# Kernel optimization log

Hardware: AMD Instinct MI355X
Metric: run time of the kernel (lower is better)

## Reference

```python
import jax, jax.numpy as jnp
import numpy as np

N, E, B, P = 131072, 262144, 4096, 1024
HID, CTX, FEAT, L = 256, 128, 512, 4


def _ln(x, g, bb, eps=1e-5):
    mu = jnp.mean(x, -1, keepdims=True)
    v = jnp.mean((x - mu) ** 2, -1, keepdims=True)
    return (x - mu) * jax.lax.rsqrt(v + eps) * g + bb


def setup_inputs() -> dict:
    key = jax.random.key(0)
    ks = iter(jax.random.split(key, 64))
    nrm = lambda sh, s=0.05: (jax.random.normal(next(ks), sh, jnp.float32) * s)
    inp = {
        "nf": jax.random.normal(next(ks), (N, 69), jnp.float32),
        "ei": jax.random.randint(next(ks), (2, E), 0, N, dtype=jnp.int32),
        "ef": jax.random.normal(next(ks), (E, 9), jnp.float32),
        "b": jnp.sort(jax.random.randint(next(ks), (N,), 0, B, dtype=jnp.int32)),
        "pid": jax.random.randint(next(ks), (B,), 0, P, dtype=jnp.int32),
        # MPNN params
        "Wn": nrm((69, HID)), "bn": jnp.zeros((HID,)),
        "We": nrm((9, HID)), "be": jnp.zeros((HID,)),
        "Wm": nrm((L, 2 * HID, HID)), "bm": jnp.zeros((L, HID)),
        "Wu": nrm((L, HID, HID)), "bu": jnp.zeros((L, HID)),
        "lng": jnp.ones((L, HID)), "lnb": jnp.zeros((L, HID)),
        # context embedding
        "ctx_emb": nrm((P, CTX), 0.02),
        # FiLM gamma net: Linear(128,256)-LN-ReLU-Linear(256,512)
        "gW1": nrm((CTX, HID)), "gb1": jnp.zeros((HID,)),
        "glng": jnp.ones((HID,)), "glnb": jnp.zeros((HID,)),
        "gW2": nrm((HID, FEAT)), "gb2": jnp.ones((FEAT,)),
        # FiLM beta net
        "bW1": nrm((CTX, HID)), "bb1": jnp.zeros((HID,)),
        "blng": jnp.ones((HID,)), "blnb": jnp.zeros((HID,)),
        "bW2": nrm((HID, FEAT)), "bb2": jnp.zeros((FEAT,)),
        # predictor: Linear(512,256)-ReLU-Linear(256,1)
        "pW1": nrm((FEAT, HID)), "pb1": jnp.zeros((HID,)),
        "pW2": nrm((HID, 1)), "pb2": jnp.zeros((1,)),
    }
    return inp


def reference(nf, ei, ef, b, pid, Wn, bn, We, be, Wm, bm, Wu, bu, lng, lnb,
              ctx_emb, gW1, gb1, glng, glnb, gW2, gb2,
              bW1, bb1, blng, blnb, bW2, bb2, pW1, pb1, pW2, pb2):
    src, dst = ei[0], ei[1]
    h = jax.nn.relu(nf @ Wn + bn)          # [N,256]
    e = jax.nn.relu(ef @ We + be)          # [E,256]
    for l in range(L):
        m = jax.nn.relu(jnp.concatenate([h[src], e], -1) @ Wm[l] + bm[l])  # [E,256]
        agg = jax.ops.segment_sum(m, dst, num_segments=N)                   # scatter-add
        h = _ln(h + jax.nn.relu(agg @ Wu[l] + bu[l]), lng[l], lnb[l])
    # graph readout: mean || max -> [B,512]
    ssum = jax.ops.segment_sum(h, b, num_segments=B)
    cnt = jnp.maximum(jax.ops.segment_sum(jnp.ones((h.shape[0], 1), h.dtype), b, num_segments=B), 1.0)
    gmax = jax.ops.segment_max(h, b, num_segments=B)
    gmax = jnp.where(jnp.isneginf(gmax), 0.0, gmax)
    g = jnp.concatenate([ssum / cnt, gmax], -1)  # [B,512]
    # FiLM fusion
    c = ctx_emb[pid]                              # [B,128]
    gamma = jax.nn.relu(_ln(c @ gW1 + gb1, glng, glnb)) @ gW2 + gb2
    beta = jax.nn.relu(_ln(c @ bW1 + bb1, blng, blnb)) @ bW2 + bb2
    hmod = gamma * g + beta
    out = (jax.nn.relu(hmod @ pW1 + pb1) @ pW2 + pb2).squeeze(-1)  # [B]
    return out
```

## Files before the change

### kernel.cpp

```cpp
#include <hip/hip_runtime.h>
#include <hip/hip_bf16.h>
#include <math.h>

#define HID 256
#define CTXD 128
#define FEAT 512
#define NLAYER 4

#define SW(n) (((n) >> 1) & 3)

typedef __hip_bfloat16 bf16;
typedef __attribute__((ext_vector_type(8))) short short8;
typedef __attribute__((ext_vector_type(4))) float floatx4;

__device__ __forceinline__ float bf2f(bf16 x) { return __bfloat162float(x); }
__device__ __forceinline__ bf16 f2bf(float x) { return __float2bfloat16(x); }
__device__ __forceinline__ float us2f(unsigned short u) {
    union { unsigned u; float f; } c; c.u = ((unsigned)u) << 16; return c.f;
}
__device__ __forceinline__ unsigned short f2us(float f) {
    bf16 b = f2bf(f); return *(unsigned short*)&b;
}

__device__ __forceinline__ void glds16(const void* g, void* l) {
    __builtin_amdgcn_global_load_lds(
        (__attribute__((address_space(1))) void*)g,
        (__attribute__((address_space(3))) void*)l, 16, 0, 0);
}

__global__ __launch_bounds__(256) void hist_kernel(const int* __restrict__ dst,
                                                   int* __restrict__ cnt, int E)
{
    int i = blockIdx.x * 256 + threadIdx.x;
    if (i < E) atomicAdd(&cnt[dst[i]], 1);
}

__global__ __launch_bounds__(256) void scan1_kernel(int* __restrict__ cnt,
                                                    int* __restrict__ bsum)
{
    __shared__ int sd[256];
    const int t = threadIdx.x;
    const int i = blockIdx.x * 256 + t;
    int v = cnt[i];
    sd[t] = v;
    __syncthreads();
    for (int o = 1; o < 256; o <<= 1) {
        int x = (t >= o) ? sd[t - o] : 0;
        __syncthreads();
        sd[t] += x;
        __syncthreads();
    }
    cnt[i] = sd[t] - v;
    if (t == 255) bsum[blockIdx.x] = sd[255];
}

__global__ void scan2_kernel(int* __restrict__ bsum)
{
    __shared__ int sd[512];
    const int t = threadIdx.x;
    int v = bsum[t];
    sd[t] = v;
    __syncthreads();
    for (int o = 1; o < 512; o <<= 1) {
        int x = (t >= o) ? sd[t - o] : 0;
        __syncthreads();
        sd[t] += x;
        __syncthreads();
    }
    bsum[t] = sd[t] - v;
}

__global__ __launch_bounds__(256) void scan3_kernel(int* __restrict__ cnt,
                                                    const int* __restrict__ bsum)
{
    int i = blockIdx.x * 256 + threadIdx.x;
    cnt[i] += bsum[blockIdx.x];
}

__global__ __launch_bounds__(256) void scatter_perm_kernel(
    const int* __restrict__ dst, int* __restrict__ cursor,
    int* __restrict__ perm, int E)
{
    int i = blockIdx.x * 256 + threadIdx.x;
    if (i < E) {
        int p = atomicAdd(&cursor[dst[i]], 1);
        perm[p] = i;
    }
}

__global__ __launch_bounds__(256)
void build_wimg_kernel(const float* __restrict__ W, bf16* __restrict__ img,
                       int K, int KT, int L)
{
    long idx = (long)blockIdx.x * 256 + threadIdx.x;
    long tot = (long)L * KT * 8192;
    if (idx >= tot) return;
    int l  = (int)(idx / ((long)KT * 8192));
    int r  = (int)(idx % ((long)KT * 8192));
    int kt = r >> 13;
    int r2 = r & 8191;
    int n  = r2 >> 5;
    int s  = (r2 >> 3) & 3;
    int j  = r2 & 7;
    int k  = kt * 32 + ((s ^ SW(n)) * 8) + j;
    float v = (k < K) ? W[((long)l * K + k) * HID + n] : 0.f;
    img[idx] = f2bf(v);
}

__device__ __forceinline__ void kt_tail512(
    int kt, const bf16* __restrict__ Wimg, const float* __restrict__ W,
    short* As, short* Bs, floatx4 (&acc)[4][4])
{
    const int t = threadIdx.x;
    const int w = t >> 6, lane = t & 63;
    const int fr = lane & 15, q = lane >> 4;
    const int wm = (w & 1) * 64, wn = (w >> 1) * 64;
    const int k0 = kt * 32;

    if (Wimg) {
        const short* base = (const short*)Wimg + (long)kt * 8192;
#pragma unroll
        for (int j = 0; j < 2; ++j) {
            const int chunk = w * 2 + j;
            glds16(base + chunk * 512 + lane * 8, (char*)Bs + chunk * 1024);
        }
    } else {
#pragma unroll
        for (int cc = 0; cc < 2; ++cc) {
            const int slot = t + cc * 512;
            const int n    = slot >> 2;
            const int kg   = slot & 3;
            const int kk   = k0 + kg * 8;
            short8 pk;
#pragma unroll
            for (int j = 0; j < 8; ++j)
                pk[j] = (short)f2us(W[(long)(kk + j) * HID + n]);
            *(short8*)&Bs[n * 32 + (kg ^ SW(n)) * 8] = pk;
        }
    }
    __syncthreads();
    short8 af[4], bf8[4];
#pragma unroll
    for (int mt = 0; mt < 4; ++mt) {
        const int r = wm + mt * 16 + fr;
        af[mt] = *(const short8*)&As[r * 32 + (q ^ SW(r)) * 8];
    }
#pragma unroll
    for (int nt = 0; nt < 4; ++nt) {
        const int r = wn + nt * 16 + fr;
        bf8[nt] = *(const short8*)&Bs[r * 32 + (q ^ SW(r)) * 8];
    }
#pragma unroll
    for (int mt = 0; mt < 4; ++mt)
#pragma unroll
        for (int nt = 0; nt < 4; ++nt)
            acc[mt][nt] = __builtin_amdgcn_mfma_f32_16x16x32_bf16(
                af[mt], bf8[nt], acc[mt][nt], 0, 0, 0);
    __syncthreads();
}

__device__ __forceinline__ void kt_tail256(
    int kt, const bf16* __restrict__ Wimg, const float* __restrict__ W,
    short* As, short* Bs, floatx4 (&acc)[4][4])
{
    const int t = threadIdx.x;
    const int w = t >> 6, lane = t & 63;
    const int fr = lane & 15, q = lane >> 4;
    const int wn = w * 64;
    const int k0 = kt * 32;

    if (Wimg) {
        const short* base = (const short*)Wimg + (long)kt * 8192;
#pragma unroll
        for (int j = 0; j < 4; ++j) {
            const int chunk = w * 4 + j;
            glds16(base + chunk * 512 + lane * 8, (char*)Bs + chunk * 1024);
        }
    } else {
#pragma unroll
        for (int cc = 0; cc < 4; ++cc) {
            const int slot = t + cc * 256;
            const int n    = slot >> 2;
            const int kg   = slot & 3;
            const int kk   = k0 + kg * 8;
            short8 pk;
#pragma unroll
            for (int j = 0; j < 8; ++j)
                pk[j] = (short)f2us(W[(long)(kk + j) * HID + n]);
            *(short8*)&Bs[n * 32 + (kg ^ SW(n)) * 8] = pk;
        }
    }
    __syncthreads();
    short8 af[4], bf8[4];
#pragma unroll
    for (int mt = 0; mt < 4; ++mt) {
        const int r = mt * 16 + fr;
        af[mt] = *(const short8*)&As[r * 32 + (q ^ SW(r)) * 8];
    }
#pragma unroll
    for (int nt = 0; nt < 4; ++nt) {
        const int r = wn + nt * 16 + fr;
        bf8[nt] = *(const short8*)&Bs[r * 32 + (q ^ SW(r)) * 8];
    }
#pragma unroll
    for (int mt = 0; mt < 4; ++mt)
#pragma unroll
        for (int nt = 0; nt < 4; ++nt)
            acc[mt][nt] = __builtin_amdgcn_mfma_f32_16x16x32_bf16(
                af[mt], bf8[nt], acc[mt][nt], 0, 0, 0);
    __syncthreads();
}

__global__ __launch_bounds__(512)
void ht_gemm(const bf16* __restrict__ h_, const float* __restrict__ W,
             const bf16* __restrict__ Wimg, bf16* __restrict__ ht)
{
    __shared__ __align__(16) short As[128 * 32];
    __shared__ __align__(16) short Bs[256 * 32];

    const int  t  = threadIdx.x;
    const long bm = (long)blockIdx.x * 128;

    floatx4 acc[4][4];
#pragma unroll
    for (int i = 0; i < 4; ++i)
#pragma unroll
        for (int j = 0; j < 4; ++j) acc[i][j] = (floatx4){0.f, 0.f, 0.f, 0.f};

    const int w = t >> 6, lane = t & 63;
    const int fr = lane & 15, q = lane >> 4;
    const int wm = (w & 1) * 64, wn = (w >> 1) * 64;
    const int arow = t >> 2, akg = t & 3;
    const int aslot = arow * 32 + (akg ^ SW(arow)) * 8;

    for (int kt = 0; kt < 8; ++kt) {
        const int kk = kt * 32 + akg * 8;
        short8 v = *(const short8*)((const short*)h_ + (bm + arow) * HID + kk);
        *(short8*)&As[aslot] = v;
        kt_tail512(kt, Wimg, W, As, Bs, acc);
    }

#pragma unroll
    for (int nt = 0; nt < 4; ++nt) {
        const int col = wn + nt * 16 + fr;
#pragma unroll
        for (int mt = 0; mt < 4; ++mt)
#pragma unroll
            for (int reg = 0; reg < 4; ++reg) {
                const long row = bm + wm + mt * 16 + q * 4 + reg;
                ht[row * HID + col] = f2bf(acc[mt][nt][reg]);
            }
    }
}

__global__ __launch_bounds__(256)
void msg_agg(const bf16* __restrict__ ht, const float* __restrict__ ef,
             const float* __restrict__ We, const float* __restrict__ be,
             const int* __restrict__ src, const int* __restrict__ perm,
             const int* __restrict__ cursor,
             const float* __restrict__ W, const bf16* __restrict__ Wimg,
             const float* __restrict__ bias, bf16* __restrict__ agg)
{
    __shared__ __align__(16) short As[64 * 32];
    __shared__ __align__(16) short Bs[256 * 32];
    __shared__ __align__(16) short htL[64 * 256];
    __shared__ int   rpL[65];
    __shared__ int   srcL[64];
    __shared__ int   edgeL[64];
    __shared__ float efL[64][9];

    const int t  = threadIdx.x;
    const int n0 = blockIdx.x * 64;

    if (t < 64) rpL[t + 1] = cursor[n0 + t];
    if (t == 0) rpL[0] = (n0 == 0) ? 0 : cursor[n0 - 1];
    __syncthreads();
    const int j0 = rpL[0], j1 = rpL[64];
    int nch = (j1 - j0 + 63) >> 6;
    if (nch < 1) nch = 1;

    const int w = t >> 6, lane = t & 63;
    const int fr = lane & 15, q = lane >> 4;
    const int wn = w * 64;
    const int arow = t >> 2, akg = t & 3;
    const int aslot = arow * 32 + (akg ^ SW(arow)) * 8;
    const int srow = t >> 2, ssg = t & 3;

    for (int ch = 0; ch < nch; ++ch) {
        const int jc = j0 + ch * 64;
        if (t < 64) {
            const int j = jc + t;
            const int eg = (j < j1) ? perm[j] : 0;
            edgeL[t] = eg;
            srcL[t]  = src[eg];
        }
        __syncthreads();
        for (int i = t; i < 64 * 9; i += 256) {
            const int r = i / 9, qq = i % 9;
            efL[r][qq] = (jc + r < j1) ? ef[(long)edgeL[r] * 9 + qq] : 0.f;
        }
        short8 stash[8];
        {
            const short* hp = (const short*)ht + (long)srcL[srow] * HID + ssg * 64;
#pragma unroll
            for (int i = 0; i < 8; ++i) stash[i] = *(const short8*)(hp + i * 8);
        }
        __syncthreads();

        floatx4 acc[4][4];
#pragma unroll
        for (int i = 0; i < 4; ++i)
#pragma unroll
            for (int j = 0; j < 4; ++j) acc[i][j] = (floatx4){0.f, 0.f, 0.f, 0.f};

        for (int kt = 0; kt < 8; ++kt) {
            const int kc = kt * 32 + akg * 8;
            float sv[8];
#pragma unroll
            for (int j = 0; j < 8; ++j) sv[j] = be[kc + j];
#pragma unroll
            for (int qq = 0; qq < 9; ++qq) {
                const float efv = efL[arow][qq];
#pragma unroll
                for (int j = 0; j < 8; ++j)
                    sv[j] = fmaf(efv, We[qq * HID + kc + j], sv[j]);
            }
            short8 pk;
#pragma unroll
            for (int j = 0; j < 8; ++j) pk[j] = (short)f2us(fmaxf(sv[j], 0.f));
            *(short8*)&As[aslot] = pk;
            kt_tail256(kt, Wimg, W, As, Bs, acc);
        }

        {
            short* hl = &htL[srow * 256 + ssg * 64];
#pragma unroll
            for (int i = 0; i < 8; ++i) *(short8*)(hl + i * 8) = stash[i];
        }
        __syncthreads();

#pragma unroll
        for (int nt = 0; nt < 4; ++nt) {
            const int col = wn + nt * 16 + fr;
            const float bv = bias[col];
#pragma unroll
            for (int mt = 0; mt < 4; ++mt)
#pragma unroll
                for (int reg = 0; reg < 4; ++reg) {
                    const int rl = mt * 16 + q * 4 + reg;
                    const float v = fmaxf(acc[mt][nt][reg] + bv +
                                          us2f((unsigned short)htL[rl * 256 + col]), 0.f);
                    htL[rl * 256 + col] = (short)f2us(v);
                }
        }
        __syncthreads();

        for (int nn = 0; nn < 16; ++nn) {
            const int nl = w * 16 + nn;
            int a = rpL[nl]     - jc; if (a < 0)  a = 0;
            int b = rpL[nl + 1] - jc; if (b > 64) b = 64;
            float s0 = 0.f, s1 = 0.f, s2 = 0.f, s3 = 0.f;
            for (int r = a; r < b; ++r) {
                const ushort4 hv = *(const ushort4*)&htL[r * 256 + lane * 4];
                s0 += us2f(hv.x); s1 += us2f(hv.y);
                s2 += us2f(hv.z); s3 += us2f(hv.w);
            }
            bf16* ap = agg + (long)(n0 + nl) * HID + lane * 4;
            if (ch == 0) {
                unsigned short o[4] = {f2us(s0), f2us(s1), f2us(s2), f2us(s3)};
                *(ushort4*)ap = *(const ushort4*)o;
            } else if (b > a) {
                const ushort4 ov = *(const ushort4*)ap;
                unsigned short o[4] = {f2us(s0 + us2f(ov.x)), f2us(s1 + us2f(ov.y)),
                                       f2us(s2 + us2f(ov.z)), f2us(s3 + us2f(ov.w))};
                *(ushort4*)ap = *(const ushort4*)o;
            }
        }
        __syncthreads();
    }
}

__global__ __launch_bounds__(512)
void upd_gemm5(const bf16* __restrict__ agg,
               const float* __restrict__ W, const bf16* __restrict__ Wimg,
               const float* __restrict__ bias,
               const float* __restrict__ lng, const float* __restrict__ lnb,
               bf16* __restrict__ h_)
{
    __shared__ __align__(16) short As[128 * 32];
    __shared__ __align__(16) short Bs[256 * 32];
    __shared__ float redS[128][4];
    __shared__ float redS2[128][4];

    const int  t  = threadIdx.x;
    const long bm = (long)blockIdx.x * 128;

    floatx4 acc[4][4];
#pragma unroll
    for (int i = 0; i < 4; ++i)
#pragma unroll
        for (int j = 0; j < 4; ++j) acc[i][j] = (floatx4){0.f, 0.f, 0.f, 0.f};

    const int w = t >> 6, lane = t & 63;
    const int fr = lane & 15, q = lane >> 4;
    const int wm = (w & 1) * 64, wn = (w >> 1) * 64;
    const int arow = t >> 2, akg = t & 3;
    const int aslot = arow * 32 + (akg ^ SW(arow)) * 8;

    for (int kt = 0; kt < 8; ++kt) {
        const int kk = kt * 32 + akg * 8;
        short8 v = *(const short8*)((const short*)agg + (bm + arow) * HID + kk);
        *(short8*)&As[aslot] = v;
        kt_tail512(kt, Wimg, W, As, Bs, acc);
    }

    const int wnIdx = w >> 1;
#pragma unroll
    for (int mt = 0; mt < 4; ++mt)
#pragma unroll
        for (int reg = 0; reg < 4; ++reg) {
            const int  lrow = wm + mt * 16 + q * 4 + reg;
            const long row  = bm + lrow;
            float ps = 0.f, ps2 = 0.f;
#pragma unroll
            for (int nt = 0; nt < 4; ++nt) {
                const int col = wn + nt * 16 + fr;
                float v = bf2f(h_[row * HID + col]) +
                          fmaxf(acc[mt][nt][reg] + bias[col], 0.f);
                acc[mt][nt][reg] = v;
                ps  += v;
                ps2 += v * v;
            }
#pragma unroll
            for (int m = 1; m < 16; m <<= 1) {
                ps  += __shfl_xor(ps, m);
                ps2 += __shfl_xor(ps2, m);
            }
            if (fr == 0) { redS[lrow][wnIdx] = ps; redS2[lrow][wnIdx] = ps2; }
        }
    __syncthreads();
#pragma unroll
    for (int mt = 0; mt < 4; ++mt)
#pragma unroll
        for (int reg = 0; reg < 4; ++reg) {
            const int  lrow = wm + mt * 16 + q * 4 + reg;
            const long row  = bm + lrow;
            const float ts  = redS[lrow][0] + redS[lrow][1] +
                              redS[lrow][2] + redS[lrow][3];
            const float ts2 = redS2[lrow][0] + redS2[lrow][1] +
                              redS2[lrow][2] + redS2[lrow][3];
            const float mu  = ts * (1.f / 256.f);
            const float var = ts2 * (1.f / 256.f) - mu * mu;
            const float rs  = rsqrtf(var + 1e-5f);
#pragma unroll
            for (int nt = 0; nt < 4; ++nt) {
                const int col = wn + nt * 16 + fr;
                const float y = (acc[mt][nt][reg] - mu) * rs * lng[col] + lnb[col];
                h_[row * HID + col] = f2bf(y);
            }
        }
}

__global__ __launch_bounds__(512)
void enc_gemm3(const float* __restrict__ nf, const bf16* __restrict__ Wimg,
               const float* __restrict__ bias, bf16* __restrict__ h_)
{
    __shared__ __align__(16) short As[128 * 32];
    __shared__ __align__(16) short Bs[256 * 32];

    const int  t  = threadIdx.x;
    const long bm = (long)blockIdx.x * 128;

    floatx4 acc[4][4];
#pragma unroll
    for (int i = 0; i < 4; ++i)
#pragma unroll
        for (int j = 0; j < 4; ++j) acc[i][j] = (floatx4){0.f, 0.f, 0.f, 0.f};

    const int w = t >> 6, lane = t & 63;
    const int fr = lane & 15, q = lane >> 4;
    const int wm = (w & 1) * 64, wn = (w >> 1) * 64;
    const int arow = t >> 2, akg = t & 3;
    const int aslot = arow * 32 + (akg ^ SW(arow)) * 8;

    for (int kt = 0; kt < 3; ++kt) {
        const int kk = kt * 32 + akg * 8;
        short8 pk;
#pragma unroll
        for (int j = 0; j < 8; ++j) {
            const int k = kk + j;
            pk[j] = (short)f2us((k < 69) ? nf[(bm + arow) * 69 + k] : 0.f);
        }
        *(short8*)&As[aslot] = pk;
        kt_tail512(kt, Wimg, nullptr, As, Bs, acc);
    }

#pragma unroll
    for (int nt = 0; nt < 4; ++nt) {
        const int col = wn + nt * 16 + fr;
        const float bv = bias[col];
#pragma unroll
        for (int mt = 0; mt < 4; ++mt)
#pragma unroll
            for (int reg = 0; reg < 4; ++reg) {
                const long row = bm + wm + mt * 16 + q * 4 + reg;
                h_[row * HID + col] = f2bf(fmaxf(acc[mt][nt][reg] + bv, 0.f));
            }
    }
}

struct PlainF32 {
    const float* A; int lda;
    __device__ float operator()(int r, int k) const { return A[(long)r * lda + k]; }
};
struct CtxF32 {
    const float* ctx; const int* pid;
    __device__ float operator()(int r, int k) const {
        return ctx[(long)pid[r] * CTXD + k];
    }
};
struct StoreF32 {
    float* C; int ldc; int relu;
    __device__ void operator()(int r, int c, const float* v) const {
        float4 o;
        o.x = v[0]; o.y = v[1]; o.z = v[2]; o.w = v[3];
        if (relu) {
            o.x = fmaxf(o.x, 0.f); o.y = fmaxf(o.y, 0.f);
            o.z = fmaxf(o.z, 0.f); o.w = fmaxf(o.w, 0.f);
        }
        *(float4*)&C[(long)r * ldc + c] = o;
    }
};
struct StoreBf16Relu {
    bf16* C;
    __device__ void operator()(int r, int c, const float* v) const {
        bf16 tmp[4];
#pragma unroll
        for (int j = 0; j < 4; ++j) tmp[j] = f2bf(fmaxf(v[j], 0.f));
        *(ushort4*)&C[(long)r * HID + c] = *(const ushort4*)tmp;
    }
};

template <typename Loader, typename Epi>
__global__ __launch_bounds__(256)
void gemm_tiled(Loader loader, const float* __restrict__ W,
                const float* __restrict__ bias, Epi epi, int M, int K, int Nc)
{
    constexpr int BM = 64, BN = 64, BK = 16;
    __shared__ __align__(16) float As[BK][BM + 4];
    __shared__ __align__(16) float Ws[BK][BN];

    const int bm = blockIdx.x * BM;
    const int bn = blockIdx.y * BN;
    const int t  = threadIdx.x;
    const int arow = t >> 2, akq = (t & 3) * 4;
    const int wn = t & 63, wk0 = t >> 6;
    const int tx = t & 15, ty = t >> 4;

    float acc[4][4] = {};
    const int ntiles = (K + BK - 1) / BK;
    for (int kt = 0; kt < ntiles; ++kt) {
        const int k0 = kt * BK;
#pragma unroll
        for (int i = 0; i < 4; ++i) {
            int k = k0 + akq + i;
            As[akq + i][arow] = (k < K) ? loader(bm + arow, k) : 0.f;
        }
#pragma unroll
        for (int i = 0; i < 4; ++i) {
            int kr = wk0 + i * 4;
            int k  = k0 + kr;
            Ws[kr][wn] = (k < K) ? W[(long)k * Nc + bn + wn] : 0.f;
        }
        __syncthreads();
#pragma unroll
        for (int kk = 0; kk < BK; ++kk) {
            float4 a = *(const float4*)&As[kk][ty * 4];
            float4 b = *(const float4*)&Ws[kk][tx * 4];
            float av[4] = {a.x, a.y, a.z, a.w};
            float bv[4] = {b.x, b.y, b.z, b.w};
#pragma unroll
            for (int i = 0; i < 4; ++i)
#pragma unroll
                for (int j = 0; j < 4; ++j) acc[i][j] += av[i] * bv[j];
        }
        __syncthreads();
    }
#pragma unroll
    for (int i = 0; i < 4; ++i) {
        const int row = bm + ty * 4 + i;
        const int col = bn + tx * 4;
        float v[4];
#pragma unroll
        for (int j = 0; j < 4; ++j) v[j] = acc[i][j] + bias[col + j];
        epi(row, col, v);
    }
}

__global__ __launch_bounds__(256)
void ln_f32_relu_kernel(float* __restrict__ x, const float* __restrict__ g,
                        const float* __restrict__ bb)
{
    const long row = blockIdx.x;
    const int  j   = threadIdx.x;
    float v = x[row * HID + j];
    float s = v, s2 = v * v;
#pragma unroll
    for (int o = 32; o > 0; o >>= 1) {
        s  += __shfl_down(s, o);
        s2 += __shfl_down(s2, o);
    }
    __shared__ float red[2][4];
    const int wid = j >> 6, lane = j & 63;
    if (lane == 0) { red[0][wid] = s; red[1][wid] = s2; }
    __syncthreads();
    float ts  = red[0][0] + red[0][1] + red[0][2] + red[0][3];
    float ts2 = red[1][0] + red[1][1] + red[1][2] + red[1][3];
    float mu  = ts * (1.f / 256.f);
    float var = ts2 * (1.f / 256.f) - mu * mu;
    float y = (v - mu) * rsqrtf(var + 1e-5f) * g[j] + bb[j];
    x[row * HID + j] = fmaxf(y, 0.f);
}

__device__ int lower_bound_i(const int* __restrict__ arr, int n, int val)
{
    int lo = 0, hi = n;
    while (lo < hi) {
        int mid = (lo + hi) >> 1;
        if (arr[mid] < val) lo = mid + 1; else hi = mid;
    }
    return lo;
}

__global__ __launch_bounds__(256)
void readout_kernel(const bf16* __restrict__ h, const int* __restrict__ b,
                    float* __restrict__ gout, int Nn)
{
    const int gidx = blockIdx.x;
    const int j    = threadIdx.x;
    const int lo   = lower_bound_i(b, Nn, gidx);
    const int hi   = lower_bound_i(b, Nn, gidx + 1);
    float s = 0.f, mx = -INFINITY;
    for (int n = lo; n < hi; ++n) {
        float v = bf2f(h[(long)n * HID + j]);
        s += v;
        mx = fmaxf(mx, v);
    }
    const int cnt = hi - lo;
    gout[(long)gidx * FEAT + j]       = s / fmaxf((float)cnt, 1.f);
    gout[(long)gidx * FEAT + HID + j] = (cnt > 0) ? mx : 0.f;
}

__global__ __launch_bounds__(256)
void film_mod_kernel(const float* __restrict__ gamma, float* __restrict__ g,
                     const float* __restrict__ beta, int n)
{
    int i = blockIdx.x * 256 + threadIdx.x;
    if (i < n) g[i] = gamma[i] * g[i] + beta[i];
}

__global__ __launch_bounds__(256)
void final_dot_kernel(const float* __restrict__ ph, const float* __restrict__ w,
                      const float* __restrict__ b2, float* __restrict__ out)
{
    const int row  = blockIdx.x * 4 + (threadIdx.x >> 6);
    const int lane = threadIdx.x & 63;
    float s = 0.f;
#pragma unroll
    for (int k = lane; k < HID; k += 64)
        s += ph[(long)row * HID + k] * w[k];
#pragma unroll
    for (int o = 32; o > 0; o >>= 1) s += __shfl_down(s, o);
    if (lane == 0) out[row] = s + b2[0];
}

__global__ void diag_out_kernel(float* out, int n, float wsmb)
{
    int i = blockIdx.x * 256 + threadIdx.x;
    if (i < n) out[i] = (i == 0) ? wsmb : 0.f;
}

extern "C" void kernel_launch(void* const* d_in, const int* in_sizes, int n_in,
                              void* d_out, int out_size, void* d_ws, size_t ws_size,
                              hipStream_t stream)
{
    const int N = 131072, E = 262144, B = 4096;

    const float* nf   = (const float*)d_in[0];
    const int*   ei   = (const int*)  d_in[1];
    const float* ef   = (const float*)d_in[2];
    const int*   bidx = (const int*)  d_in[3];
    const int*   pid  = (const int*)  d_in[4];
    const float* Wn   = (const float*)d_in[5];
    const float* bn   = (const float*)d_in[6];
    const float* We   = (const float*)d_in[7];
    const float* be   = (const float*)d_in[8];
    const float* Wm   = (const float*)d_in[9];
    const float* bm   = (const float*)d_in[10];
    const float* Wu   = (const float*)d_in[11];
    const float* bu   = (const float*)d_in[12];
    const float* lng  = (const float*)d_in[13];
    const float* lnb  = (const float*)d_in[14];
    const float* ctx  = (const float*)d_in[15];
    const float* gW1  = (const float*)d_in[16];
    const float* gb1  = (const float*)d_in[17];
    const float* glng = (const float*)d_in[18];
    const float* glnb = (const float*)d_in[19];
    const float* gW2  = (const float*)d_in[20];
    const float* gb2  = (const float*)d_in[21];
    const float* bW1  = (const float*)d_in[22];
    const float* bb1  = (const float*)d_in[23];
    const float* blng = (const float*)d_in[24];
    const float* blnb = (const float*)d_in[25];
    const float* bW2  = (const float*)d_in[26];
    const float* bb2  = (const float*)d_in[27];
    const float* pW1  = (const float*)d_in[28];
    const float* pb1  = (const float*)d_in[29];
    const float* pW2  = (const float*)d_in[30];
    const float* pb2  = (const float*)d_in[31];

    const int* src = ei;
    const int* dst = ei + E;
    float* out = (float*)d_out;

    const size_t hB    = (size_t)N * HID * sizeof(bf16);
    const size_t htB   = (size_t)N * HID * sizeof(bf16);
    const size_t aggB  = (size_t)N * HID * sizeof(bf16);
    const size_t curB  = (size_t)N * 4;
    const size_t permB = (size_t)E * 4;
    const size_t bsumB = 2048 * 4;
    const size_t wmImgB = (size_t)NLAYER * 16 * 8192 * 2;
    const size_t wuImgB = (size_t)NLAYER * 8  * 8192 * 2;
    const size_t wnImgB = (size_t)3 * 8192 * 2;

    const size_t needBase = hB + htB + aggB + curB + permB + bsumB;
    const size_t needFull = needBase + wmImgB + wuImgB + wnImgB;

    if (ws_size < needBase) {
        diag_out_kernel<<<dim3((B + 255) / 256), dim3(256), 0, stream>>>(
            out, B, (float)(ws_size >> 20));
        return;
    }
    const bool haveImg = ws_size >= needFull;

    char* p = (char*)d_ws;
    bf16* h      = (bf16*)p;  p += hB;
    bf16* ht     = (bf16*)p;  p += htB;
    bf16* agg    = (bf16*)p;  p += aggB;
    int*  cursor = (int*)p;   p += curB;
    int*  perm   = (int*)p;   p += permB;
    int*  bsum   = (int*)p;   p += bsumB;
    bf16* wmImg = nullptr; bf16* wuImg = nullptr; bf16* wnImg = nullptr;
    if (haveImg) {
        wmImg = (bf16*)p; p += wmImgB;
        wuImg = (bf16*)p; p += wuImgB;
        wnImg = (bf16*)p; p += wnImgB;
    }

    float* gbuf  = (float*)ht;
    float* t1    = gbuf  + (long)B * FEAT;
    float* t2    = t1    + (long)B * HID;
    float* gamma = t2    + (long)B * HID;
    float* beta  = gamma + (long)B * FEAT;
    float* ph    = beta  + (long)B * FEAT;

    dim3 blk(256), blk5(512);

    hipMemsetAsync(cursor, 0, curB, stream);
    hist_kernel<<<dim3(E / 256), blk, 0, stream>>>(dst, cursor, E);
    scan1_kernel<<<dim3(N / 256), blk, 0, stream>>>(cursor, bsum);
    scan2_kernel<<<dim3(1), dim3(512), 0, stream>>>(bsum);
    scan3_kernel<<<dim3(N / 256), blk, 0, stream>>>(cursor, bsum);
    scatter_perm_kernel<<<dim3(E / 256), blk, 0, stream>>>(dst, cursor, perm, E);

    if (haveImg) {
        build_wimg_kernel<<<dim3((NLAYER * 16 * 8192 + 255) / 256), blk, 0, stream>>>(
            Wm, wmImg, 2 * HID, 16, NLAYER);
        build_wimg_kernel<<<dim3((NLAYER * 8 * 8192 + 255) / 256), blk, 0, stream>>>(
            Wu, wuImg, HID, 8, NLAYER);
        build_wimg_kernel<<<dim3((3 * 8192 + 255) / 256), blk, 0, stream>>>(
            Wn, wnImg, 69, 3, 1);
    }

    if (haveImg) {
        enc_gemm3<<<dim3(N / 128), blk5, 0, stream>>>(nf, wnImg, bn, h);
    } else {
        gemm_tiled<<<dim3(N / 64, HID / 64), blk, 0, stream>>>(
            PlainF32{nf, 69}, Wn, bn, StoreBf16Relu{h}, N, 69, HID);
    }

    for (int l = 0; l < NLAYER; ++l) {
        const float* Wml  = Wm  + (long)l * 2 * HID * HID;
        const float* WmlB = Wml + (long)HID * HID;
        const float* bml  = bm  + (long)l * HID;
        const float* Wul  = Wu  + (long)l * HID * HID;
        const float* bul  = bu  + (long)l * HID;
        const float* lngl = lng + (long)l * HID;
        const float* lnbl = lnb + (long)l * HID;
        const bf16* wmTopI = haveImg ? wmImg + (long)l * 16 * 8192 : nullptr;
        const bf16* wmBotI = haveImg ? wmImg + (long)l * 16 * 8192 + 8 * 8192 : nullptr;
        const bf16* wuI    = haveImg ? wuImg + (long)l * 8 * 8192 : nullptr;

        ht_gemm<<<dim3(N / 128), blk5, 0, stream>>>(h, Wml, wmTopI, ht);
        msg_agg<<<dim3(N / 64), blk, 0, stream>>>(
            ht, ef, We, be, src, perm, cursor, WmlB, wmBotI, bml, agg);
        upd_gemm5<<<dim3(N / 128), blk5, 0, stream>>>(
            agg, Wul, wuI, bul, lngl, lnbl, h);
    }

    readout_kernel<<<dim3(B), blk, 0, stream>>>(h, bidx, gbuf, N);

    gemm_tiled<<<dim3(B / 64, HID / 64), blk, 0, stream>>>(
        CtxF32{ctx, pid}, gW1, gb1, StoreF32{t1, HID, 0}, B, CTXD, HID);
    ln_f32_relu_kernel<<<dim3(B), blk, 0, stream>>>(t1, glng, glnb);
    gemm_tiled<<<dim3(B / 64, FEAT / 64), blk, 0, stream>>>(
        PlainF32{t1, HID}, gW2, gb2, StoreF32{gamma, FEAT, 0}, B, HID, FEAT);

    gemm_tiled<<<dim3(B / 64, HID / 64), blk, 0, stream>>>(
        CtxF32{ctx, pid}, bW1, bb1, StoreF32{t2, HID, 0}, B, CTXD, HID);
    ln_f32_relu_kernel<<<dim3(B), blk, 0, stream>>>(t2, blng, blnb);
    gemm_tiled<<<dim3(B / 64, FEAT / 64), blk, 0, stream>>>(
        PlainF32{t2, HID}, bW2, bb2, StoreF32{beta, FEAT, 0}, B, HID, FEAT);

    film_mod_kernel<<<dim3((B * FEAT + 255) / 256), blk, 0, stream>>>(
        gamma, gbuf, beta, B * FEAT);
    gemm_tiled<<<dim3(B / 64, HID / 64), blk, 0, stream>>>(
        PlainF32{gbuf, FEAT}, pW1, pb1, StoreF32{ph, HID, 1}, B, FEAT, HID);
    final_dot_kernel<<<dim3(B / 4), blk, 0, stream>>>(ph, pW2, pb2, out);
}
```

Baseline: 2.146 ms.

## Restructure message kernel to read bottom weights directly from global memory

Adds msg_agg2, which computes the full 64x256 edge-embedding tile into a single swizzled LDS buffer up front. The MFMA loop then runs over all k-tiles, loading B fragments straight from a new plain (unswizzled) bf16 weight image in global/L2, instead of staging weights through LDS with per-k-tile barriers. The shared buffer is then reused for the gathered ht rows and the aggregation. This cuts LDS traffic and synchronisation per chunk, at the cost of register-direct global loads of weights and an extra weight-build kernel.

```diff
diff --git a/kernel.cpp b/kernel.cpp
--- a/kernel.cpp
+++ b/kernel.cpp
@@ -26,6 +26,10 @@
     __builtin_amdgcn_global_load_lds(
         (__attribute__((address_space(1))) void*)g,
         (__attribute__((address_space(3))) void*)l, 16, 0, 0);
+}
+
+__device__ __forceinline__ int hsw(int row, int col) {
+    return row * 256 + ((((col) >> 3) ^ (row & 31)) << 3) + ((col) & 7);
 }
 
 __global__ __launch_bounds__(256) void hist_kernel(const int* __restrict__ dst,
@@ -107,6 +111,23 @@
     img[idx] = f2bf(v);
 }
 
+__global__ __launch_bounds__(256)
+void build_wbot_plain_kernel(const float* __restrict__ Wm, bf16* __restrict__ img)
+{
+    long idx = (long)blockIdx.x * 256 + threadIdx.x;
+    long tot = (long)NLAYER * 8 * 8192;
+    if (idx >= tot) return;
+    int l  = (int)(idx / (8 * 8192));
+    int r  = (int)(idx % (8 * 8192));
+    int kt = r >> 13;
+    int r2 = r & 8191;
+    int n  = r2 >> 5;
+    int kc = r2 & 31;
+    int k  = 256 + kt * 32 + kc;
+    img[(long)l * 16 * 8192 + (long)(8 + kt) * 8192 + n * 32 + kc] =
+        f2bf(Wm[((long)l * 512 + k) * HID + n]);
+}
+
 __device__ __forceinline__ void kt_tail512(
     int kt, const bf16* __restrict__ Wimg, const float* __restrict__ W,
     short* As, short* Bs, floatx4 (&acc)[4][4])
@@ -159,8 +180,195 @@
     __syncthreads();
 }
 
+__global__ __launch_bounds__(512)
+void ht_gemm(const bf16* __restrict__ h_, const float* __restrict__ W,
+             const bf16* __restrict__ Wimg, bf16* __restrict__ ht)
+{
+    __shared__ __align__(16) short As[128 * 32];
+    __shared__ __align__(16) short Bs[256 * 32];
+
+    const int  t  = threadIdx.x;
+    const long bm = (long)blockIdx.x * 128;
+
+    floatx4 acc[4][4];
+#pragma unroll
+    for (int i = 0; i < 4; ++i)
+#pragma unroll
+        for (int j = 0; j < 4; ++j) acc[i][j] = (floatx4){0.f, 0.f, 0.f, 0.f};
+
+    const int w = t >> 6, lane = t & 63;
+    const int fr = lane & 15, q = lane >> 4;
+    const int wm = (w & 1) * 64, wn = (w >> 1) * 64;
+    const int arow = t >> 2, akg = t & 3;
+    const int aslot = arow * 32 + (akg ^ SW(arow)) * 8;
+
+    for (int kt = 0; kt < 8; ++kt) {
+        const int kk = kt * 32 + akg * 8;
+        short8 v = *(const short8*)((const short*)h_ + (bm + arow) * HID + kk);
+        *(short8*)&As[aslot] = v;
+        kt_tail512(kt, Wimg, W, As, Bs, acc);
+    }
+
+#pragma unroll
+    for (int nt = 0; nt < 4; ++nt) {
+        const int col = wn + nt * 16 + fr;
+#pragma unroll
+        for (int mt = 0; mt < 4; ++mt)
+#pragma unroll
+            for (int reg = 0; reg < 4; ++reg) {
+                const long row = bm + wm + mt * 16 + q * 4 + reg;
+                ht[row * HID + col] = f2bf(acc[mt][nt][reg]);
+            }
+    }
+}
+
+__global__ __launch_bounds__(256)
+void msg_agg2(const bf16* __restrict__ ht, const float* __restrict__ ef,
+              const float* __restrict__ We, const float* __restrict__ be,
+              const int* __restrict__ src, const int* __restrict__ perm,
+              const int* __restrict__ cursor,
+              const bf16* __restrict__ WbP,
+              const float* __restrict__ bias, bf16* __restrict__ agg)
+{
+    __shared__ __align__(16) short vL[64 * 256];
+    __shared__ int   rpL[65];
+    __shared__ int   srcL[64];
+    __shared__ int   edgeL[64];
+    __shared__ float efL[64][9];
+
+    const int t  = threadIdx.x;
+    const int n0 = blockIdx.x * 64;
+
+    if (t < 64) rpL[t + 1] = cursor[n0 + t];
+    if (t == 0) rpL[0] = (n0 == 0) ? 0 : cursor[n0 - 1];
+    __syncthreads();
+    const int j0 = rpL[0], j1 = rpL[64];
+    int nch = (j1 - j0 + 63) >> 6;
+    if (nch < 1) nch = 1;
+
+    const int w = t >> 6, lane = t & 63;
+    const int fr = lane & 15, q = lane >> 4;
+    const int wn = w * 64;
+    const int row = t >> 2, sg = t & 3;
+
+    for (int ch = 0; ch < nch; ++ch) {
+        const int jc = j0 + ch * 64;
+        if (t < 64) {
+            const int j = jc + t;
+            const int eg = (j < j1) ? perm[j] : 0;
+            edgeL[t] = eg;
+            srcL[t]  = src[eg];
+        }
+        __syncthreads();
+        for (int i = t; i < 64 * 9; i += 256) {
+            const int r = i / 9, qq = i % 9;
+            efL[r][qq] = (jc + r < j1) ? ef[(long)edgeL[r] * 9 + qq] : 0.f;
+        }
+        short8 stash[8];
+        {
+            const short* hp = (const short*)ht + (long)srcL[row] * HID + sg * 64;
+#pragma unroll
+            for (int i = 0; i < 8; ++i) stash[i] = *(const short8*)(hp + i * 8);
+        }
+        __syncthreads();
+
+#pragma unroll
+        for (int i = 0; i < 8; ++i) {
+            const int c0 = sg * 64 + i * 8;
+            float sv[8];
+#pragma unroll
+            for (int j = 0; j < 8; ++j) sv[j] = be[c0 + j];
+#pragma unroll
+            for (int qq = 0; qq < 9; ++qq) {
+                const float efv = efL[row][qq];
+#pragma unroll
+                for (int j = 0; j < 8; ++j)
+                    sv[j] = fmaf(efv, We[qq * HID + c0 + j], sv[j]);
+            }
+            short8 pk;
+#pragma unroll
+            for (int j = 0; j < 8; ++j) pk[j] = (short)f2us(fmaxf(sv[j], 0.f));
+            *(short8*)&vL[hsw(row, c0)] = pk;
+        }
+        __syncthreads();
+
+        floatx4 acc[4][4];
+#pragma unroll
+        for (int i = 0; i < 4; ++i)
+#pragma unroll
+            for (int j = 0; j < 4; ++j) acc[i][j] = (floatx4){0.f, 0.f, 0.f, 0.f};
+
+#pragma unroll 2
+        for (int kt = 0; kt < 8; ++kt) {
+            short8 bfv[4], af[4];
+#pragma unroll
+            for (int nt = 0; nt < 4; ++nt)
+                bfv[nt] = *(const short8*)((const short*)WbP + (long)kt * 8192 +
+                                           (wn + nt * 16 + fr) * 32 + q * 8);
+#pragma unroll
+            for (int mt = 0; mt < 4; ++mt)
+                af[mt] = *(const short8*)&vL[hsw(mt * 16 + fr, kt * 32 + q * 8)];
+#pragma unroll
+            for (int mt = 0; mt < 4; ++mt)
+#pragma unroll
+                for (int nt = 0; nt < 4; ++nt)
+                    acc[mt][nt] = __builtin_amdgcn_mfma_f32_16x16x32_bf16(
+                        af[mt], bfv[nt], acc[mt][nt], 0, 0, 0);
+        }
+        __syncthreads();
+
+        {
+            const int c0 = sg * 64;
+#pragma unroll
+            for (int i = 0; i < 8; ++i)
+                *(short8*)&vL[hsw(row, c0 + i * 8)] = stash[i];
+        }
+        __syncthreads();
+
+#pragma unroll
+        for (int nt = 0; nt < 4; ++nt) {
+            const int col = wn + nt * 16 + fr;
+            const float bv = bias[col];
+#pragma unroll
+            for (int mt = 0; mt < 4; ++mt)
+#pragma unroll
+                for (int reg = 0; reg < 4; ++reg) {
+                    const int rl = mt * 16 + q * 4 + reg;
+                    const int a  = hsw(rl, col);
+                    const float v = fmaxf(acc[mt][nt][reg] + bv +
+                                          us2f((unsigned short)vL[a]), 0.f);
+                    vL[a] = (short)f2us(v);
+                }
+        }
+        __syncthreads();
+
+        for (int nn = 0; nn < 16; ++nn) {
+            const int nl = w * 16 + nn;
+            int a = rpL[nl]     - jc; if (a < 0)  a = 0;
+            int b = rpL[nl + 1] - jc; if (b > 64) b = 64;
+            float s0 = 0.f, s1 = 0.f, s2 = 0.f, s3 = 0.f;
+            for (int r = a; r < b; ++r) {
+                const ushort4 hv = *(const ushort4*)&vL[hsw(r, lane * 4)];
+                s0 += us2f(hv.x); s1 += us2f(hv.y);
+                s2 += us2f(hv.z); s3 += us2f(hv.w);
+            }
+            bf16* ap = agg + (long)(n0 + nl) * HID + lane * 4;
+            if (ch == 0) {
+                unsigned short o[4] = {f2us(s0), f2us(s1), f2us(s2), f2us(s3)};
+                *(ushort4*)ap = *(const ushort4*)o;
+            } else if (b > a) {
+                const ushort4 ov = *(const ushort4*)ap;
+                unsigned short o[4] = {f2us(s0 + us2f(ov.x)), f2us(s1 + us2f(ov.y)),
+                                       f2us(s2 + us2f(ov.z)), f2us(s3 + us2f(ov.w))};
+                *(ushort4*)ap = *(const ushort4*)o;
+            }
+        }
+        __syncthreads();
+    }
+}
+
 __device__ __forceinline__ void kt_tail256(
-    int kt, const bf16* __restrict__ Wimg, const float* __restrict__ W,
+    int kt, const float* __restrict__ W,
     short* As, short* Bs, floatx4 (&acc)[4][4])
 {
     const int t = threadIdx.x;
@@ -169,26 +377,17 @@
     const int wn = w * 64;
     const int k0 = kt * 32;
 
-    if (Wimg) {
-        const short* base = (const short*)Wimg + (long)kt * 8192;
-#pragma unroll
-        for (int j = 0; j < 4; ++j) {
-            const int chunk = w * 4 + j;
-            glds16(base + chunk * 512 + lane * 8, (char*)Bs + chunk * 1024);
-        }
-    } else {
-#pragma unroll
-        for (int cc = 0; cc < 4; ++cc) {
-            const int slot = t + cc * 256;
-            const int n    = slot >> 2;
-            const int kg   = slot & 3;
-            const int kk   = k0 + kg * 8;
-            short8 pk;
-#pragma unroll
-            for (int j = 0; j < 8; ++j)
-                pk[j] = (short)f2us(W[(long)(kk + j) * HID + n]);
-            *(short8*)&Bs[n * 32 + (kg ^ SW(n)) * 8] = pk;
-        }
+#pragma unroll
+    for (int cc = 0; cc < 4; ++cc) {
+        const int slot = t + cc * 256;
+        const int n    = slot >> 2;
+        const int kg   = slot & 3;
+        const int kk   = k0 + kg * 8;
+        short8 pk;
+#pragma unroll
+        for (int j = 0; j < 8; ++j)
+            pk[j] = (short)f2us(W[(long)(kk + j) * HID + n]);
+        *(short8*)&Bs[n * 32 + (kg ^ SW(n)) * 8] = pk;
     }
     __syncthreads();
     short8 af[4], bf8[4];
@@ -211,55 +410,13 @@
     __syncthreads();
 }
 
-__global__ __launch_bounds__(512)
-void ht_gemm(const bf16* __restrict__ h_, const float* __restrict__ W,
-             const bf16* __restrict__ Wimg, bf16* __restrict__ ht)
-{
-    __shared__ __align__(16) short As[128 * 32];
-    __shared__ __align__(16) short Bs[256 * 32];
-
-    const int  t  = threadIdx.x;
-    const long bm = (long)blockIdx.x * 128;
-
-    floatx4 acc[4][4];
-#pragma unroll
-    for (int i = 0; i < 4; ++i)
-#pragma unroll
-        for (int j = 0; j < 4; ++j) acc[i][j] = (floatx4){0.f, 0.f, 0.f, 0.f};
-
-    const int w = t >> 6, lane = t & 63;
-    const int fr = lane & 15, q = lane >> 4;
-    const int wm = (w & 1) * 64, wn = (w >> 1) * 64;
-    const int arow = t >> 2, akg = t & 3;
-    const int aslot = arow * 32 + (akg ^ SW(arow)) * 8;
-
-    for (int kt = 0; kt < 8; ++kt) {
-        const int kk = kt * 32 + akg * 8;
-        short8 v = *(const short8*)((const short*)h_ + (bm + arow) * HID + kk);
-        *(short8*)&As[aslot] = v;
-        kt_tail512(kt, Wimg, W, As, Bs, acc);
-    }
-
-#pragma unroll
-    for (int nt = 0; nt < 4; ++nt) {
-        const int col = wn + nt * 16 + fr;
-#pragma unroll
-        for (int mt = 0; mt < 4; ++mt)
-#pragma unroll
-            for (int reg = 0; reg < 4; ++reg) {
-                const long row = bm + wm + mt * 16 + q * 4 + reg;
-                ht[row * HID + col] = f2bf(acc[mt][nt][reg]);
-            }
-    }
-}
-
 __global__ __launch_bounds__(256)
-void msg_agg(const bf16* __restrict__ ht, const float* __restrict__ ef,
-             const float* __restrict__ We, const float* __restrict__ be,
-             const int* __restrict__ src, const int* __restrict__ perm,
-             const int* __restrict__ cursor,
-             const float* __restrict__ W, const bf16* __restrict__ Wimg,
-             const float* __restrict__ bias, bf16* __restrict__ agg)
+void msg_agg_fb(const bf16* __restrict__ ht, const float* __restrict__ ef,
+                const float* __restrict__ We, const float* __restrict__ be,
+                const int* __restrict__ src, const int* __restrict__ perm,
+                const int* __restrict__ cursor,
+                const float* __restrict__ W,
+                const float* __restrict__ bias, bf16* __restrict__ agg)
 {
     __shared__ __align__(16) short As[64 * 32];
     __shared__ __align__(16) short Bs[256 * 32];
@@ -329,13 +486,14 @@
 #pragma unroll
             for (int j = 0; j < 8; ++j) pk[j] = (short)f2us(fmaxf(sv[j], 0.f));
             *(short8*)&As[aslot] = pk;
-            kt_tail256(kt, Wimg, W, As, Bs, acc);
+            kt_tail256(kt, W, As, Bs, acc);
         }
 
         {
-            short* hl = &htL[srow * 256 + ssg * 64];
-#pragma unroll
-            for (int i = 0; i < 8; ++i) *(short8*)(hl + i * 8) = stash[i];
+            const int c0 = ssg * 64;
+#pragma unroll
+            for (int i = 0; i < 8; ++i)
+                *(short8*)&htL[hsw(srow, c0 + i * 8)] = stash[i];
         }
         __syncthreads();
 
@@ -348,9 +506,10 @@
 #pragma unroll
                 for (int reg = 0; reg < 4; ++reg) {
                     const int rl = mt * 16 + q * 4 + reg;
+                    const int a  = hsw(rl, col);
                     const float v = fmaxf(acc[mt][nt][reg] + bv +
-                                          us2f((unsigned short)htL[rl * 256 + col]), 0.f);
-                    htL[rl * 256 + col] = (short)f2us(v);
+                                          us2f((unsigned short)htL[a]), 0.f);
+                    htL[a] = (short)f2us(v);
                 }
         }
         __syncthreads();
@@ -361,7 +520,7 @@
             int b = rpL[nl + 1] - jc; if (b > 64) b = 64;
             float s0 = 0.f, s1 = 0.f, s2 = 0.f, s3 = 0.f;
             for (int r = a; r < b; ++r) {
-                const ushort4 hv = *(const ushort4*)&htL[r * 256 + lane * 4];
+                const ushort4 hv = *(const ushort4*)&htL[hsw(r, lane * 4)];
                 s0 += us2f(hv.x); s1 += us2f(hv.y);
                 s2 += us2f(hv.z); s3 += us2f(hv.w);
             }
@@ -776,6 +935,8 @@
     if (haveImg) {
         build_wimg_kernel<<<dim3((NLAYER * 16 * 8192 + 255) / 256), blk, 0, stream>>>(
             Wm, wmImg, 2 * HID, 16, NLAYER);
+        build_wbot_plain_kernel<<<dim3((NLAYER * 8 * 8192 + 255) / 256), blk, 0, stream>>>(
+            Wm, wmImg);
         build_wimg_kernel<<<dim3((NLAYER * 8 * 8192 + 255) / 256), blk, 0, stream>>>(
             Wu, wuImg, HID, 8, NLAYER);
         build_wimg_kernel<<<dim3((3 * 8192 + 255) / 256), blk, 0, stream>>>(
@@ -798,12 +959,17 @@
         const float* lngl = lng + (long)l * HID;
         const float* lnbl = lnb + (long)l * HID;
         const bf16* wmTopI = haveImg ? wmImg + (long)l * 16 * 8192 : nullptr;
-        const bf16* wmBotI = haveImg ? wmImg + (long)l * 16 * 8192 + 8 * 8192 : nullptr;
+        const bf16* wbPlain = haveImg ? wmImg + (long)l * 16 * 8192 + 8 * 8192 : nullptr;
         const bf16* wuI    = haveImg ? wuImg + (long)l * 8 * 8192 : nullptr;
 
         ht_gemm<<<dim3(N / 128), blk5, 0, stream>>>(h, Wml, wmTopI, ht);
-        msg_agg<<<dim3(N / 64), blk, 0, stream>>>(
-            ht, ef, We, be, src, perm, cursor, WmlB, wmBotI, bml, agg);
+        if (haveImg) {
+            msg_agg2<<<dim3(N / 64), blk, 0, stream>>>(
+                ht, ef, We, be, src, perm, cursor, wbPlain, bml, agg);
+        } else {
+            msg_agg_fb<<<dim3(N / 64), blk, 0, stream>>>(
+                ht, ef, We, be, src, perm, cursor, WmlB, bml, agg);
+        }
         upd_gemm5<<<dim3(N / 128), blk5, 0, stream>>>(
             agg, Wul, wuI, bul, lngl, lnbl, h);
     }
```

Result: slower. 5.489 ms (+155.8%).
